# Kernel optimization log

Hardware: AMD Instinct MI355X
Metric: run time of the kernel (lower is better)

The kernel has to match this reference:

```python
import jax, jax.numpy as jnp
import numpy as np

N_FEAT = 7          # input_vector_size
M = 3               # memberships per feature (hardcoded 3 in torch module)
FUZZ = M ** N_FEAT  # 2187, cartesian product size
MID = 512
NUM_CLASS = 10
BATCH = 4096

# Precompute cartesian-product index table: itertools.product over rows of u[i]
# (last feature index varies fastest). IDX[k, i] = which of the 3 memberships of
# feature i appears in combination k.
_k = np.arange(FUZZ)
IDX = ((_k[:, None] // (M ** np.arange(N_FEAT - 1, -1, -1))[None, :]) % M).astype(np.int32)  # [FUZZ, N_FEAT]


def setup_inputs() -> dict:
    key = jax.random.key(0)
    ks = jax.random.split(key, 8)
    x = jax.random.normal(ks[0], (BATCH, N_FEAT), dtype=jnp.float32)
    # Parameters (xavier-ish init for weights, ones for b/bais as in torch init)
    c = jax.random.uniform(ks[1], (N_FEAT, M), minval=-1.0, maxval=1.0, dtype=jnp.float32)
    b = jnp.ones((N_FEAT, M), dtype=jnp.float32)
    wei = jax.random.uniform(ks[2], (FUZZ * N_FEAT, FUZZ), minval=-0.01, maxval=0.01, dtype=jnp.float32)
    bais = jnp.ones((1,), dtype=jnp.float32)
    W1 = jax.random.normal(ks[3], (MID, FUZZ), dtype=jnp.float32) * (1.0 / np.sqrt(FUZZ))
    b1 = jnp.zeros((MID,), dtype=jnp.float32)
    W2 = jax.random.normal(ks[4], (FUZZ, MID), dtype=jnp.float32) * (1.0 / np.sqrt(MID))
    b2 = jnp.zeros((FUZZ,), dtype=jnp.float32)
    W3 = jax.random.normal(ks[5], (NUM_CLASS, FUZZ), dtype=jnp.float32) * (1.0 / np.sqrt(FUZZ))
    b3 = jnp.zeros((NUM_CLASS,), dtype=jnp.float32)
    return {"x": x, "c": c, "b": b, "wei": wei, "bais": bais,
            "W1": W1, "b1": b1, "W2": W2, "b2": b2, "W3": W3, "b3": b3}


def reference(x, c, b, wei, bais, W1, b1, W2, b2, W3, b3):
    B = x.shape[0]
    # Gaussian fuzzy memberships: u[b, i, j] = exp(-(x[b,i]-c[i,j])^2 / b[i,j]^2)
    u = jnp.exp(-((x[:, :, None] - c[None]) ** 2) / (b[None] ** 2))  # [B, N_FEAT, M]
    # Cartesian product: dd[bt, k, i] = u[bt, i, IDX[k, i]]  (replaces itertools.product)
    idx = jnp.asarray(IDX)                       # [FUZZ, N_FEAT]
    feat = jnp.arange(N_FEAT)[None, :]           # [1, N_FEAT] broadcasts to [FUZZ, N_FEAT]
    dd = u[:, feat, idx]                         # [B, FUZZ, N_FEAT]
    # Fuzzy rule layer
    a = dd.reshape(B, FUZZ * N_FEAT) @ wei + bais            # [B, FUZZ]
    a_mean = a / jnp.sum(a, axis=1, keepdims=True)
    # Small residual MLP
    h1 = a_mean @ W1.T + b1                                   # [B, MID]
    h2 = h1 @ W2.T + b2                                       # [B, FUZZ]
    h3 = (a_mean + h2) @ W3.T + b3                            # [B, NUM_CLASS]
    out = jax.nn.leaky_relu(h3, negative_slope=0.2)
    # Dropout(0.5) omitted (eval mode / deterministic baseline)
    return out
```

## Files before the change

### kernel.cpp

```cpp
#include <hip/hip_runtime.h>

#define FUZZ 2187
#define NFEAT 7
#define MID 512
#define NCLS 10
#define BATCH 4096
#define SSTR 2192

__global__ __launch_bounds__(256) void k_reduce_wei(const float* __restrict__ wei,
                                                    float* __restrict__ S) {
    int n = blockIdx.x * 256 + threadIdx.x;
    if (n >= FUZZ) return;
    int by = blockIdx.y;
    int t = by;
    int d4 = t % 3; t /= 3;
    int d3 = t % 3; t /= 3;
    int d2 = t % 3; t /= 3;
    int d1 = t % 3; t /= 3;
    int d0 = t;
    float a0 = 0.f, a1 = 0.f, a2 = 0.f, a3 = 0.f, a4 = 0.f;
    float h5[3] = {0.f, 0.f, 0.f};
    float h6[3] = {0.f, 0.f, 0.f};
    const float* base = wei + (size_t)(by * 63) * FUZZ + n;
#pragma unroll
    for (int kk = 0; kk < 9; ++kk) {
        const float* rowp = base + (size_t)(kk * 7) * FUZZ;
        float v0 = rowp[0];
        float v1 = rowp[(size_t)1 * FUZZ];
        float v2 = rowp[(size_t)2 * FUZZ];
        float v3 = rowp[(size_t)3 * FUZZ];
        float v4 = rowp[(size_t)4 * FUZZ];
        float v5 = rowp[(size_t)5 * FUZZ];
        float v6 = rowp[(size_t)6 * FUZZ];
        a0 += v0; a1 += v1; a2 += v2; a3 += v3; a4 += v4;
        h5[kk / 3] += v5;
        h6[kk % 3] += v6;
    }
    atomicAdd(&S[(0  + d0) * SSTR + n], a0);
    atomicAdd(&S[(3  + d1) * SSTR + n], a1);
    atomicAdd(&S[(6  + d2) * SSTR + n], a2);
    atomicAdd(&S[(9  + d3) * SSTR + n], a3);
    atomicAdd(&S[(12 + d4) * SSTR + n], a4);
#pragma unroll
    for (int m = 0; m < 3; ++m) {
        atomicAdd(&S[(15 + m) * SSTR + n], h5[m]);
        atomicAdd(&S[(18 + m) * SSTR + n], h6[m]);
    }
}

__device__ __forceinline__ float wave_sum(float v) {
#pragma unroll
    for (int off = 32; off > 0; off >>= 1) v += __shfl_down(v, off, 64);
    return v;
}

__global__ __launch_bounds__(256) void k_sw1(const float* __restrict__ S,
                                             const float* __restrict__ W1,
                                             float* __restrict__ SW1,
                                             float* __restrict__ ws1) {
    int i = blockIdx.x;
    int tid = threadIdx.x;
    float acc[21];
    float aw = 0.f;
#pragma unroll
    for (int t = 0; t < 21; ++t) acc[t] = 0.f;
    const float* w1row = W1 + (size_t)i * FUZZ;
    for (int n = tid; n < FUZZ; n += 256) {
        float w1 = w1row[n];
        aw += w1;
#pragma unroll
        for (int t = 0; t < 21; ++t) acc[t] += S[t * SSTR + n] * w1;
    }
#pragma unroll
    for (int t = 0; t < 21; ++t) acc[t] = wave_sum(acc[t]);
    aw = wave_sum(aw);
    __shared__ float red[4][22];
    int w = tid >> 6, lane = tid & 63;
    if (lane == 0) {
#pragma unroll
        for (int t = 0; t < 21; ++t) red[w][t] = acc[t];
        red[w][21] = aw;
    }
    __syncthreads();
    if (tid < 22) {
        float s = red[0][tid] + red[1][tid] + red[2][tid] + red[3][tid];
        if (tid < 21) SW1[tid * MID + i] = s;
        else          ws1[i] = s;
    }
}

__global__ __launch_bounds__(128) void k_g(const float* __restrict__ SW1,
                                           const float* __restrict__ ws1,
                                           const float* __restrict__ b1,
                                           const float* __restrict__ W2,
                                           float* __restrict__ G,
                                           float* __restrict__ q,
                                           float* __restrict__ p,
                                           float* __restrict__ THvw) {
    int n = blockIdx.x;
    int tid = threadIdx.x;
    if (n == 0 && tid < 128) {
        THvw[tid] = 0.f;
        THvw[tid + 128] = 0.f;
        if (tid < 32) THvw[tid + 256] = 0.f;
    }
    float acc[21];
    float aq = 0.f, ap = 0.f;
#pragma unroll
    for (int t = 0; t < 21; ++t) acc[t] = 0.f;
    const float* w2row = W2 + (size_t)n * MID;
    for (int i = tid; i < MID; i += 128) {
        float w2 = w2row[i];
        aq += ws1[i] * w2;
        ap += b1[i] * w2;
#pragma unroll
        for (int t = 0; t < 21; ++t) acc[t] += SW1[t * MID + i] * w2;
    }
#pragma unroll
    for (int t = 0; t < 21; ++t) acc[t] = wave_sum(acc[t]);
    aq = wave_sum(aq);
    ap = wave_sum(ap);
    __shared__ float red[2][23];
    int w = tid >> 6, lane = tid & 63;
    if (lane == 0) {
#pragma unroll
        for (int t = 0; t < 21; ++t) red[w][t] = acc[t];
        red[w][21] = aq;
        red[w][22] = ap;
    }
    __syncthreads();
    if (tid < 23) {
        float s = red[0][tid] + red[1][tid];
        if (tid < 21)      G[tid * SSTR + n] = s;
        else if (tid == 21) q[n] = s;
        else                p[n] = s;
    }
}

__global__ __launch_bounds__(64) void k_h(const float* __restrict__ S,
                                          const float* __restrict__ G,
                                          const float* __restrict__ q,
                                          const float* __restrict__ p,
                                          const float* __restrict__ b2,
                                          const float* __restrict__ b3,
                                          const float* __restrict__ W3,
                                          float* __restrict__ H,
                                          float* __restrict__ v,
                                          float* __restrict__ w,
                                          float* __restrict__ T) {
    int c = blockIdx.x;
    int chunk = blockIdx.y;
    int lane = threadIdx.x;
    int n0 = chunk * 81;
    if (c < NCLS) {
        float acc[21];
        float av = 0.f, aw = 0.f;
#pragma unroll
        for (int t = 0; t < 21; ++t) acc[t] = 0.f;
        for (int n = n0 + lane; n < n0 + 81; n += 64) {
            float w3 = W3[(size_t)c * FUZZ + n];
            av += (1.0f + q[n]) * w3;
            aw += (p[n] + b2[n]) * w3;
#pragma unroll
            for (int t = 0; t < 21; ++t)
                acc[t] += (S[t * SSTR + n] + G[t * SSTR + n]) * w3;
        }
#pragma unroll
        for (int t = 0; t < 21; ++t) acc[t] = wave_sum(acc[t]);
        av = wave_sum(av);
        aw = wave_sum(aw);
        if (lane == 0) {
#pragma unroll
            for (int t = 0; t < 21; ++t) atomicAdd(&H[t * NCLS + c], acc[t]);
            atomicAdd(&v[c], av);
            atomicAdd(&w[c], aw + (chunk == 0 ? b3[c] : 0.f));
        }
    } else {
        float acc[21];
#pragma unroll
        for (int t = 0; t < 21; ++t) acc[t] = 0.f;
        for (int n = n0 + lane; n < n0 + 81; n += 64) {
#pragma unroll
            for (int t = 0; t < 21; ++t) acc[t] += S[t * SSTR + n];
        }
#pragma unroll
        for (int t = 0; t < 21; ++t) acc[t] = wave_sum(acc[t]);
        if (lane == 0) {
#pragma unroll
            for (int t = 0; t < 21; ++t) atomicAdd(&T[t], acc[t]);
        }
    }
}

__global__ __launch_bounds__(64) void k_out(const float* __restrict__ x,
                                            const float* __restrict__ cc,
                                            const float* __restrict__ bbv,
                                            const float* __restrict__ bais,
                                            const float* __restrict__ T,
                                            const float* __restrict__ H,
                                            const float* __restrict__ v,
                                            const float* __restrict__ w,
                                            float* __restrict__ out) {
    int b = blockIdx.x * 64 + threadIdx.x;
    if (b >= BATCH) return;
    float xv[NFEAT];
#pragma unroll
    for (int j = 0; j < NFEAT; ++j) xv[j] = x[b * NFEAT + j];
    float u[21];
#pragma unroll
    for (int j = 0; j < NFEAT; ++j) {
#pragma unroll
        for (int m = 0; m < 3; ++m) {
            float d = xv[j] - cc[j * 3 + m];
            float bv = bbv[j * 3 + m];
            u[j * 3 + m] = expf(-(d * d) / (bv * bv));
        }
    }
    float ba = bais[0];
    float r = 2187.0f * ba;
#pragma unroll
    for (int t = 0; t < 21; ++t) r += u[t] * T[t];
    float inv = 1.0f / r;
#pragma unroll
    for (int c = 0; c < NCLS; ++c) {
        float s = 0.f;
#pragma unroll
        for (int t = 0; t < 21; ++t) s += u[t] * H[t * NCLS + c];
        float h = (s + ba * v[c]) * inv + w[c];
        out[b * NCLS + c] = (h >= 0.f) ? h : 0.2f * h;
    }
}

extern "C" void kernel_launch(void* const* d_in, const int* in_sizes, int n_in,
                              void* d_out, int out_size, void* d_ws, size_t ws_size,
                              hipStream_t stream) {
    const float* x    = (const float*)d_in[0];
    const float* c    = (const float*)d_in[1];
    const float* bbv  = (const float*)d_in[2];
    const float* wei  = (const float*)d_in[3];
    const float* bais = (const float*)d_in[4];
    const float* W1   = (const float*)d_in[5];
    const float* b1   = (const float*)d_in[6];
    const float* W2   = (const float*)d_in[7];
    const float* b2   = (const float*)d_in[8];
    const float* W3   = (const float*)d_in[9];
    const float* b3   = (const float*)d_in[10];

    float* ws  = (float*)d_ws;
    float* S   = ws;
    float* G   = S + 21 * SSTR;
    float* SW1 = G + 21 * SSTR;
    float* ws1 = SW1 + 21 * MID;
    float* q   = ws1 + MID;
    float* p   = q + SSTR;
    float* T   = p + SSTR;
    float* H   = T + 32;
    float* v   = H + 224;
    float* w   = v + 16;

    hipMemsetAsync(S, 0, (size_t)(21 * SSTR) * sizeof(float), stream);
    k_reduce_wei<<<dim3(9, 243), 256, 0, stream>>>(wei, S);
    k_sw1<<<MID, 256, 0, stream>>>(S, W1, SW1, ws1);
    k_g<<<FUZZ, 128, 0, stream>>>(SW1, ws1, b1, W2, G, q, p, T);
    k_h<<<dim3(NCLS + 1, 27), 64, 0, stream>>>(S, G, q, p, b2, b3, W3, H, v, w, T);
    k_out<<<(BATCH + 63) / 64, 64, 0, stream>>>(x, c, bbv, bais, T, H, v, w,
                                                (float*)d_out);
}
```

Before: 275.2 us.

## Fold W2 into W3 via precomputed K = W3·W2 and drop the k_g kernel

The product W3·W2 (10x512) is now computed in extra blocks of the k_sw1 kernel, so the per-FUZZ G/q/p projection through W2 (a 2187-block kernel) is no longer needed. k_h then combines S with W3 directly and adds the SW1·K contribution over MID, using fewer and larger chunks. This removes one launch and the 21x2187 G intermediate. In exchange, the 10 extra blocks in k_sw1 each walk 2187 rows of W2 serially, which could stretch that kernel's critical path.

```diff
diff --git a/kernel.cpp b/kernel.cpp
--- a/kernel.cpp
+++ b/kernel.cpp
@@ -56,10 +56,33 @@
 
 __global__ __launch_bounds__(256) void k_sw1(const float* __restrict__ S,
                                              const float* __restrict__ W1,
+                                             const float* __restrict__ W2,
+                                             const float* __restrict__ W3,
                                              float* __restrict__ SW1,
-                                             float* __restrict__ ws1) {
-    int i = blockIdx.x;
+                                             float* __restrict__ ws1,
+                                             float* __restrict__ K,
+                                             float* __restrict__ THvw) {
+    int gid = blockIdx.x;
     int tid = threadIdx.x;
+    if (gid >= MID) {
+        int c = gid - MID;
+        if (c == 0) {
+            THvw[tid] = 0.f;
+            if (tid < 32) THvw[tid + 256] = 0.f;
+        }
+        float acc0 = 0.f, acc1 = 0.f;
+        const float* w3row = W3 + (size_t)c * FUZZ;
+        const float* w2col = W2 + tid;
+        for (int n = 0; n < FUZZ; ++n) {
+            float w3 = w3row[n];
+            acc0 += w3 * w2col[(size_t)n * MID];
+            acc1 += w3 * w2col[(size_t)n * MID + 256];
+        }
+        K[c * MID + tid]       = acc0;
+        K[c * MID + tid + 256] = acc1;
+        return;
+    }
+    int i = gid;
     float acc[21];
     float aw = 0.f;
 #pragma unroll
@@ -89,58 +112,11 @@
     }
 }
 
-__global__ __launch_bounds__(128) void k_g(const float* __restrict__ SW1,
-                                           const float* __restrict__ ws1,
-                                           const float* __restrict__ b1,
-                                           const float* __restrict__ W2,
-                                           float* __restrict__ G,
-                                           float* __restrict__ q,
-                                           float* __restrict__ p,
-                                           float* __restrict__ THvw) {
-    int n = blockIdx.x;
-    int tid = threadIdx.x;
-    if (n == 0 && tid < 128) {
-        THvw[tid] = 0.f;
-        THvw[tid + 128] = 0.f;
-        if (tid < 32) THvw[tid + 256] = 0.f;
-    }
-    float acc[21];
-    float aq = 0.f, ap = 0.f;
-#pragma unroll
-    for (int t = 0; t < 21; ++t) acc[t] = 0.f;
-    const float* w2row = W2 + (size_t)n * MID;
-    for (int i = tid; i < MID; i += 128) {
-        float w2 = w2row[i];
-        aq += ws1[i] * w2;
-        ap += b1[i] * w2;
-#pragma unroll
-        for (int t = 0; t < 21; ++t) acc[t] += SW1[t * MID + i] * w2;
-    }
-#pragma unroll
-    for (int t = 0; t < 21; ++t) acc[t] = wave_sum(acc[t]);
-    aq = wave_sum(aq);
-    ap = wave_sum(ap);
-    __shared__ float red[2][23];
-    int w = tid >> 6, lane = tid & 63;
-    if (lane == 0) {
-#pragma unroll
-        for (int t = 0; t < 21; ++t) red[w][t] = acc[t];
-        red[w][21] = aq;
-        red[w][22] = ap;
-    }
-    __syncthreads();
-    if (tid < 23) {
-        float s = red[0][tid] + red[1][tid];
-        if (tid < 21)      G[tid * SSTR + n] = s;
-        else if (tid == 21) q[n] = s;
-        else                p[n] = s;
-    }
-}
-
 __global__ __launch_bounds__(64) void k_h(const float* __restrict__ S,
-                                          const float* __restrict__ G,
-                                          const float* __restrict__ q,
-                                          const float* __restrict__ p,
+                                          const float* __restrict__ SW1,
+                                          const float* __restrict__ ws1,
+                                          const float* __restrict__ K,
+                                          const float* __restrict__ b1,
                                           const float* __restrict__ b2,
                                           const float* __restrict__ b3,
                                           const float* __restrict__ W3,
@@ -151,19 +127,29 @@
     int c = blockIdx.x;
     int chunk = blockIdx.y;
     int lane = threadIdx.x;
-    int n0 = chunk * 81;
+    int n0 = chunk * 243;
     if (c < NCLS) {
         float acc[21];
         float av = 0.f, aw = 0.f;
 #pragma unroll
         for (int t = 0; t < 21; ++t) acc[t] = 0.f;
-        for (int n = n0 + lane; n < n0 + 81; n += 64) {
-            float w3 = W3[(size_t)c * FUZZ + n];
-            av += (1.0f + q[n]) * w3;
-            aw += (p[n] + b2[n]) * w3;
+        const float* w3row = W3 + (size_t)c * FUZZ;
+        for (int n = n0 + lane; n < n0 + 243; n += 64) {
+            float w3 = w3row[n];
+            av += w3;
+            aw += b2[n] * w3;
 #pragma unroll
             for (int t = 0; t < 21; ++t)
-                acc[t] += (S[t * SSTR + n] + G[t * SSTR + n]) * w3;
+                acc[t] += S[t * SSTR + n] * w3;
+        }
+        if (chunk < 8) {
+            int i = chunk * 64 + lane;
+            float kk = K[c * MID + i];
+            av += ws1[i] * kk;
+            aw += b1[i] * kk;
+#pragma unroll
+            for (int t = 0; t < 21; ++t)
+                acc[t] += SW1[t * MID + i] * kk;
         }
 #pragma unroll
         for (int t = 0; t < 21; ++t) acc[t] = wave_sum(acc[t]);
@@ -179,7 +165,7 @@
         float acc[21];
 #pragma unroll
         for (int t = 0; t < 21; ++t) acc[t] = 0.f;
-        for (int n = n0 + lane; n < n0 + 81; n += 64) {
+        for (int n = n0 + lane; n < n0 + 243; n += 64) {
 #pragma unroll
             for (int t = 0; t < 21; ++t) acc[t] += S[t * SSTR + n];
         }
@@ -248,21 +234,19 @@
 
     float* ws  = (float*)d_ws;
     float* S   = ws;
-    float* G   = S + 21 * SSTR;
-    float* SW1 = G + 21 * SSTR;
+    float* SW1 = S + 21 * SSTR;
     float* ws1 = SW1 + 21 * MID;
-    float* q   = ws1 + MID;
-    float* p   = q + SSTR;
-    float* T   = p + SSTR;
+    float* K   = ws1 + MID;
+    float* T   = K + NCLS * MID;
     float* H   = T + 32;
     float* v   = H + 224;
     float* w   = v + 16;
 
     hipMemsetAsync(S, 0, (size_t)(21 * SSTR) * sizeof(float), stream);
     k_reduce_wei<<<dim3(9, 243), 256, 0, stream>>>(wei, S);
-    k_sw1<<<MID, 256, 0, stream>>>(S, W1, SW1, ws1);
-    k_g<<<FUZZ, 128, 0, stream>>>(SW1, ws1, b1, W2, G, q, p, T);
-    k_h<<<dim3(NCLS + 1, 27), 64, 0, stream>>>(S, G, q, p, b2, b3, W3, H, v, w, T);
+    k_sw1<<<MID + NCLS, 256, 0, stream>>>(S, W1, W2, W3, SW1, ws1, K, T);
+    k_h<<<dim3(NCLS + 1, 9), 64, 0, stream>>>(S, SW1, ws1, K, b1, b2, b3, W3,
+                                              H, v, w, T);
     k_out<<<(BATCH + 63) / 64, 64, 0, stream>>>(x, c, bbv, bais, T, H, v, w,
                                                 (float*)d_out);
 }
```

New measurement: 384.5 us. +39.7%, slower.
